# Kernel tuning notes

Measured on AMD Instinct MI355X. Metric: run time of the kernel, lower is better.

The kernel has to match this reference:

```python
import jax, jax.numpy as jnp
import numpy as np

B, N, M, D = 4, 1024, 1024, 64


def setup_inputs() -> dict:
    key = jax.random.key(0)
    k1, k2 = jax.random.split(key)
    lhs = jax.random.normal(k1, (B, N, D), dtype=jnp.float32)
    rhs = jax.random.normal(k2, (B, M, D), dtype=jnp.float32)
    return {"lhs": lhs, "rhs": rhs}


def reference(lhs, rhs):
    # SAD similarity: -sum_d |lhs[b,n,d] - rhs[b,m,d]|  -> [B, N, M]
    # Faithful to the torch module's broadcasted abs-diff reduction.
    diff = lhs[:, :, None, :] - rhs[:, None, :, :]  # [B, N, M, D]
    similarity = -jnp.abs(diff).sum(axis=-1)        # [B, N, M]
    return similarity
```

## Files before the change

### kernel.cpp

```cpp
#include <hip/hip_runtime.h>

#define BB 4
#define NN 1024
#define MM 1024
#define DD 64
#define TN 128
#define TM 64
#define PADU 72

#define QSCALE 4096.0f
#define QBIAS  32768.5f

__device__ __forceinline__ unsigned sad16(unsigned a, unsigned b, unsigned c) {
#if __has_builtin(__builtin_amdgcn_sad_u16)
    return __builtin_amdgcn_sad_u16(a, b, c);
#else
    unsigned d;
    asm("v_sad_u16 %0, %1, %2, %3" : "=v"(d) : "v"(a), "v"(b), "v"(c));
    return d;
#endif
}

__device__ __forceinline__ unsigned q2(float lo, float hi) {
    unsigned a = (unsigned)fmaf(lo, QSCALE, QBIAS);
    unsigned b = (unsigned)fmaf(hi, QSCALE, QBIAS);
    return a | (b << 16);
}

__global__ __launch_bounds__(256, 2)
void SADSimilarity_38706245272206_kernel(const float* __restrict__ lhs,
                                         const float* __restrict__ rhs,
                                         float* __restrict__ out) {
    __shared__ unsigned short lt[TN * PADU];
    __shared__ unsigned short rt[TM * PADU];

    const int b   = blockIdx.z;
    const int n0  = blockIdx.y * TN;
    const int m0  = blockIdx.x * TM;
    const int tid = threadIdx.x;

    const float* lbase = lhs + ((size_t)b * NN + n0) * DD;
    const float* rbase = rhs + ((size_t)b * MM + m0) * DD;

    #pragma unroll
    for (int p = 0; p < 4; ++p) {
        int e   = tid + p * 256;
        int row = e >> 3;
        int c8  = (e & 7) << 3;
        const float* g = lbase + row * DD + c8;
        float4 a = *(const float4*)(g);
        float4 c = *(const float4*)(g + 4);
        uint4 w;
        w.x = q2(a.x, a.y); w.y = q2(a.z, a.w);
        w.z = q2(c.x, c.y); w.w = q2(c.z, c.w);
        *(uint4*)(&lt[row * PADU + c8]) = w;
    }
    #pragma unroll
    for (int p = 0; p < 2; ++p) {
        int e   = tid + p * 256;
        int row = e >> 3;
        int c8  = (e & 7) << 3;
        const float* g = rbase + row * DD + c8;
        float4 a = *(const float4*)(g);
        float4 c = *(const float4*)(g + 4);
        uint4 w;
        w.x = q2(a.x, a.y); w.y = q2(a.z, a.w);
        w.z = q2(c.x, c.y); w.w = q2(c.z, c.w);
        *(uint4*)(&rt[row * PADU + c8]) = w;
    }
    __syncthreads();

    const int tx = tid & 15;
    const int ty = tid >> 4;

    unsigned acc[8][4];
    #pragma unroll
    for (int i = 0; i < 8; ++i)
        #pragma unroll
        for (int j = 0; j < 4; ++j) acc[i][j] = 0u;

    #pragma unroll
    for (int dq = 0; dq < 8; ++dq) {
        uint4 l[8], r[4];
        #pragma unroll
        for (int i = 0; i < 8; ++i)
            l[i] = *(const uint4*)(&lt[(ty + 16 * i) * PADU + dq * 8]);
        #pragma unroll
        for (int j = 0; j < 4; ++j)
            r[j] = *(const uint4*)(&rt[(tx + 16 * j) * PADU + dq * 8]);
        #pragma unroll
        for (int i = 0; i < 8; ++i)
            #pragma unroll
            for (int j = 0; j < 4; ++j) {
                acc[i][j] = sad16(l[i].x, r[j].x, acc[i][j]);
                acc[i][j] = sad16(l[i].y, r[j].y, acc[i][j]);
                acc[i][j] = sad16(l[i].z, r[j].z, acc[i][j]);
                acc[i][j] = sad16(l[i].w, r[j].w, acc[i][j]);
            }
    }

    float* obase = out + (size_t)b * NN * MM + (size_t)n0 * MM + m0;
    #pragma unroll
    for (int i = 0; i < 8; ++i) {
        int row = ty + 16 * i;
        #pragma unroll
        for (int j = 0; j < 4; ++j) {
            obase[(size_t)row * MM + tx + 16 * j] = (float)acc[i][j] * (-1.0f / QSCALE);
        }
    }
}

extern "C" void kernel_launch(void* const* d_in, const int* in_sizes, int n_in,
                              void* d_out, int out_size, void* d_ws, size_t ws_size,
                              hipStream_t stream) {
    const float* lhs = (const float*)d_in[0];
    const float* rhs = (const float*)d_in[1];
    float* out = (float*)d_out;

    dim3 grid(MM / TM, NN / TN, BB);
    dim3 block(256, 1, 1);
    SADSimilarity_38706245272206_kernel<<<grid, block, 0, stream>>>(lhs, rhs, out);
}
```

Before: 67.41 us.

## Use 64x64 tiles with single-wavefront blocks and 8x8 per-thread outputs

Changes the block tile from 128x64 with 256 threads to 64x64 with 64 threads. Each thread now computes an 8x8 output micro-tile instead of 8x4, which raises register reuse of LDS operands per sad instruction, and the grid grows to 1024 blocks. The staging loop now loads lhs and rhs together with float4 granularity. In exchange the blocks are tiny single wavefronts, so the doubled accumulators may raise register pressure, and output stores are spread with a stride of 8 columns, which gives less coalescing.

```diff
diff --git a/kernel.cpp b/kernel.cpp
--- a/kernel.cpp
+++ b/kernel.cpp
@@ -4,8 +4,7 @@
 #define NN 1024
 #define MM 1024
 #define DD 64
-#define TN 128
-#define TM 64
+#define TT 64
 #define PADU 72
 
 #define QSCALE 4096.0f
@@ -27,71 +26,58 @@
     return a | (b << 16);
 }
 
-__global__ __launch_bounds__(256, 2)
+__global__ __launch_bounds__(64, 2)
 void SADSimilarity_38706245272206_kernel(const float* __restrict__ lhs,
                                          const float* __restrict__ rhs,
                                          float* __restrict__ out) {
-    __shared__ unsigned short lt[TN * PADU];
-    __shared__ unsigned short rt[TM * PADU];
+    __shared__ unsigned short lt[TT * PADU];
+    __shared__ unsigned short rt[TT * PADU];
 
     const int b   = blockIdx.z;
-    const int n0  = blockIdx.y * TN;
-    const int m0  = blockIdx.x * TM;
+    const int n0  = blockIdx.y * TT;
+    const int m0  = blockIdx.x * TT;
     const int tid = threadIdx.x;
 
     const float* lbase = lhs + ((size_t)b * NN + n0) * DD;
     const float* rbase = rhs + ((size_t)b * MM + m0) * DD;
 
     #pragma unroll
-    for (int p = 0; p < 4; ++p) {
-        int e   = tid + p * 256;
-        int row = e >> 3;
-        int c8  = (e & 7) << 3;
-        const float* g = lbase + row * DD + c8;
-        float4 a = *(const float4*)(g);
-        float4 c = *(const float4*)(g + 4);
-        uint4 w;
-        w.x = q2(a.x, a.y); w.y = q2(a.z, a.w);
-        w.z = q2(c.x, c.y); w.w = q2(c.z, c.w);
-        *(uint4*)(&lt[row * PADU + c8]) = w;
-    }
-    #pragma unroll
-    for (int p = 0; p < 2; ++p) {
-        int e   = tid + p * 256;
-        int row = e >> 3;
-        int c8  = (e & 7) << 3;
-        const float* g = rbase + row * DD + c8;
-        float4 a = *(const float4*)(g);
-        float4 c = *(const float4*)(g + 4);
-        uint4 w;
-        w.x = q2(a.x, a.y); w.y = q2(a.z, a.w);
-        w.z = q2(c.x, c.y); w.w = q2(c.z, c.w);
-        *(uint4*)(&rt[row * PADU + c8]) = w;
+    for (int p = 0; p < 16; ++p) {
+        int e   = tid + p * 64;
+        int row = e >> 4;
+        int q   = (e & 15) << 2;
+        float4 a = *(const float4*)(lbase + row * DD + q);
+        float4 c = *(const float4*)(rbase + row * DD + q);
+        uint2 wa, wc;
+        wa.x = q2(a.x, a.y); wa.y = q2(a.z, a.w);
+        wc.x = q2(c.x, c.y); wc.y = q2(c.z, c.w);
+        *(uint2*)(&lt[row * PADU + q]) = wa;
+        *(uint2*)(&rt[row * PADU + q]) = wc;
     }
     __syncthreads();
 
-    const int tx = tid & 15;
-    const int ty = tid >> 4;
+    const int tx = tid & 7;
+    const int ty = tid >> 3;
 
-    unsigned acc[8][4];
+    unsigned acc[8][8];
     #pragma unroll
     for (int i = 0; i < 8; ++i)
         #pragma unroll
-        for (int j = 0; j < 4; ++j) acc[i][j] = 0u;
+        for (int j = 0; j < 8; ++j) acc[i][j] = 0u;
 
     #pragma unroll
     for (int dq = 0; dq < 8; ++dq) {
-        uint4 l[8], r[4];
+        uint4 l[8], r[8];
         #pragma unroll
         for (int i = 0; i < 8; ++i)
-            l[i] = *(const uint4*)(&lt[(ty + 16 * i) * PADU + dq * 8]);
+            l[i] = *(const uint4*)(&lt[(ty + 8 * i) * PADU + dq * 8]);
         #pragma unroll
-        for (int j = 0; j < 4; ++j)
-            r[j] = *(const uint4*)(&rt[(tx + 16 * j) * PADU + dq * 8]);
+        for (int j = 0; j < 8; ++j)
+            r[j] = *(const uint4*)(&rt[(tx + 8 * j) * PADU + dq * 8]);
         #pragma unroll
         for (int i = 0; i < 8; ++i)
             #pragma unroll
-            for (int j = 0; j < 4; ++j) {
+            for (int j = 0; j < 8; ++j) {
                 acc[i][j] = sad16(l[i].x, r[j].x, acc[i][j]);
                 acc[i][j] = sad16(l[i].y, r[j].y, acc[i][j]);
                 acc[i][j] = sad16(l[i].z, r[j].z, acc[i][j]);
@@ -102,10 +88,10 @@
     float* obase = out + (size_t)b * NN * MM + (size_t)n0 * MM + m0;
     #pragma unroll
     for (int i = 0; i < 8; ++i) {
-        int row = ty + 16 * i;
+        int row = ty + 8 * i;
         #pragma unroll
-        for (int j = 0; j < 4; ++j) {
-            obase[(size_t)row * MM + tx + 16 * j] = (float)acc[i][j] * (-1.0f / QSCALE);
+        for (int j = 0; j < 8; ++j) {
+            obase[(size_t)row * MM + tx + 8 * j] = (float)acc[i][j] * (-1.0f / QSCALE);
         }
     }
 }
@@ -117,7 +103,7 @@
     const float* rhs = (const float*)d_in[1];
     float* out = (float*)d_out;
 
-    dim3 grid(MM / TM, NN / TN, BB);
-    dim3 block(256, 1, 1);
+    dim3 grid(MM / TT, NN / TT, BB);
+    dim3 block(64, 1, 1);
     SADSimilarity_38706245272206_kernel<<<grid, block, 0, stream>>>(lhs, rhs, out);
 }
```

Measured after the change: 68.85 us. 1.02x slower.
